# Optimization experiments

Hardware: AMD Instinct MI355X
Metric: run time of the kernel (lower is better)

## Reference

```python
import jax, jax.numpy as jnp
import numpy as np

B, IN, H = 8192, 1024, 1024


def setup_inputs() -> dict:
    key = jax.random.key(0)
    ks = jax.random.split(key, 16)
    s_in = 1.0 / np.sqrt(IN)
    s_h = 1.0 / np.sqrt(H)
    d = {}
    d['x'] = jax.random.normal(ks[0], (B, IN), jnp.float32)
    d['h'] = jax.random.normal(ks[1], (B, H), jnp.float32)
    d['c_prev'] = jax.random.normal(ks[2], (B, H), jnp.float32)
    d['W_fx'] = jax.random.normal(ks[3], (H, IN), jnp.float32) * s_in
    d['b_f'] = jax.random.normal(ks[4], (H,), jnp.float32) * s_in
    d['W_fh'] = jax.random.normal(ks[5], (H, H), jnp.float32) * s_h
    d['W_ix'] = jax.random.normal(ks[6], (H, IN), jnp.float32) * s_in
    d['b_i'] = jax.random.normal(ks[7], (H,), jnp.float32) * s_in
    d['W_ih'] = jax.random.normal(ks[8], (H, H), jnp.float32) * s_h
    d['W_gx'] = jax.random.normal(ks[9], (H, IN), jnp.float32) * s_in
    d['b_g'] = jax.random.normal(ks[10], (H,), jnp.float32) * s_in
    d['W_gh'] = jax.random.normal(ks[11], (H, H), jnp.float32) * s_h
    d['W_ox'] = jax.random.normal(ks[12], (H, IN), jnp.float32) * s_in
    d['b_o'] = jax.random.normal(ks[13], (H,), jnp.float32) * s_in
    d['W_oh'] = jax.random.normal(ks[14], (H, H), jnp.float32) * s_h
    return d


def reference(x, h, c_prev, W_fx, b_f, W_fh, W_ix, b_i, W_ih,
              W_gx, b_g, W_gh, W_ox, b_o, W_oh):
    # Concatenate the four x-projections and four h-projections into two
    # fused GEMMs (same math as the 8 separate nn.Linear calls).
    Wx = jnp.concatenate([W_ix, W_fx, W_gx, W_ox], axis=0)  # [4H, IN]
    Wh = jnp.concatenate([W_ih, W_fh, W_gh, W_oh], axis=0)  # [4H, H]
    bx = jnp.concatenate([b_i, b_f, b_g, b_o], axis=0)       # [4H]
    z = x @ Wx.T + h @ Wh.T + bx                              # [B, 4H]
    zi, zf, zg, zo = jnp.split(z, 4, axis=-1)
    i = jax.nn.sigmoid(zi)
    f = jax.nn.sigmoid(zf)
    g = jnp.tanh(zg)
    o = jax.nn.sigmoid(zo)
    c_next = f * c_prev + i * g
    h_next = o * jnp.tanh(c_next)
    return (h_next, c_next)
```

## Files before the change

kernel.cpp:

```cpp
#include <hip/hip_runtime.h>
#include <stdint.h>

typedef unsigned short ushort_t;
typedef __attribute__((ext_vector_type(8))) short short8;
typedef __attribute__((ext_vector_type(4))) float floatx4;

#define B_   8192
#define IN_  1024
#define H_   1024

#define XB_ELEMS   (B_ * IN_)
#define WB_ELEMS   (H_ * IN_)
#define WS_XB   0
#define WS_HB   XB_ELEMS
#define WS_WB   (2 * XB_ELEMS)

__device__ __forceinline__ ushort_t f2bf(float f) {
    union { float f; uint32_t i; } v; v.f = f;
    uint32_t r = (v.i + 0x7fffu + ((v.i >> 16) & 1u)) >> 16;
    return (ushort_t)r;
}
__device__ __forceinline__ float sigmoid_(float x) {
    return 1.0f / (1.0f + __expf(-x));
}
__device__ __forceinline__ float tanh_(float x) {
    float xc = fminf(fmaxf(x, -20.f), 20.f);
    float e = __expf(2.f * xc);
    return (e - 1.f) / (e + 1.f);
}

__device__ __forceinline__ void gll16(const ushort_t* gsrc, ushort_t* ldst) {
    __builtin_amdgcn_global_load_lds(
        (const __attribute__((address_space(1))) void*)gsrc,
        (__attribute__((address_space(3))) void*)ldst,
        16, 0, 0);
}

__global__ __launch_bounds__(256) void cvt_kernel(
    const float* __restrict__ X,   const float* __restrict__ Hin,
    const float* __restrict__ Wix, const float* __restrict__ Wfx,
    const float* __restrict__ Wgx, const float* __restrict__ Wox,
    const float* __restrict__ Wih, const float* __restrict__ Wfh,
    const float* __restrict__ Wgh, const float* __restrict__ Woh,
    ushort_t* __restrict__ ws)
{
    const int c = blockIdx.x * 256 + threadIdx.x;
    const float* src;
    ushort_t* dst;
    int off;
    if (c < 2097152) {
        const int t = c >> 20;
        src = t ? Hin : X;
        dst = ws + (t ? WS_HB : WS_XB);
        off = (c & 1048575) * 8;
    } else {
        const int cc = c - 2097152;
        const int s = cc >> 17;
        const float* w =
            s == 0 ? Wix : s == 1 ? Wfx : s == 2 ? Wgx : s == 3 ? Wox :
            s == 4 ? Wih : s == 5 ? Wfh : s == 6 ? Wgh : Woh;
        src = w;
        dst = ws + WS_WB + s * WB_ELEMS;
        off = (cc & 131071) * 8;
    }
    float4 f0 = *(const float4*)(src + off);
    float4 f1 = *(const float4*)(src + off + 4);
    short8 o;
    o[0] = (short)f2bf(f0.x); o[1] = (short)f2bf(f0.y);
    o[2] = (short)f2bf(f0.z); o[3] = (short)f2bf(f0.w);
    o[4] = (short)f2bf(f1.x); o[5] = (short)f2bf(f1.y);
    o[6] = (short)f2bf(f1.z); o[7] = (short)f2bf(f1.w);
    *(short8*)(dst + off) = o;
}

__global__ __launch_bounds__(256) void lstm_cell_kernel(
    const ushort_t* __restrict__ Xb,  const ushort_t* __restrict__ Hb,
    const ushort_t* __restrict__ Wb,
    const float* __restrict__ Cprev,
    const float* __restrict__ Bi, const float* __restrict__ Bf,
    const float* __restrict__ Bg, const float* __restrict__ Bo,
    float* __restrict__ Out)
{
    __shared__ __align__(16) ushort_t As[128 * 32];
    __shared__ __align__(16) ushort_t Bs[128 * 32];

    const int t   = threadIdx.x;
    const int bm0 = blockIdx.y * 128;
    const int j0  = blockIdx.x * 32;

    const int idx0 = t, idx1 = t + 256;
    const int rA0 = idx0 >> 2, kA0 = (idx0 & 3) * 8;
    const int rA1 = idx1 >> 2, kA1 = (idx1 & 3) * 8;

    const ushort_t* xA0 = Xb + (size_t)(bm0 + rA0) * IN_ + kA0;
    const ushort_t* xA1 = Xb + (size_t)(bm0 + rA1) * IN_ + kA1;
    const ushort_t* hA0 = Hb + (size_t)(bm0 + rA0) * H_  + kA0;
    const ushort_t* hA1 = Hb + (size_t)(bm0 + rA1) * H_  + kA1;

    const int g0 = (rA0 >> 4) & 3, g1 = (rA1 >> 4) & 3;
    const int jj0_ = j0 + ((rA0 >> 6) << 4) + (rA0 & 15);
    const int jj1_ = j0 + ((rA1 >> 6) << 4) + (rA1 & 15);
    const ushort_t* wx0 = Wb + (size_t)g0 * WB_ELEMS + (size_t)jj0_ * IN_ + kA0;
    const ushort_t* wx1 = Wb + (size_t)g1 * WB_ELEMS + (size_t)jj1_ * IN_ + kA1;
    const ushort_t* wh0 = Wb + (size_t)(4 + g0) * WB_ELEMS + (size_t)jj0_ * H_ + kA0;
    const ushort_t* wh1 = Wb + (size_t)(4 + g1) * WB_ELEMS + (size_t)jj1_ * H_ + kA1;

    ushort_t* ldsA0 = &As[idx0 * 8];
    ushort_t* ldsA1 = &As[idx1 * 8];
    ushort_t* ldsB0 = &Bs[idx0 * 8];
    ushort_t* ldsB1 = &Bs[idx1 * 8];

    const int lane = t & 63;
    const int w = t >> 6;
    const int lr = lane & 15, lk = lane >> 4;
    const int rowbase = (w >> 1) * 64;
    const int colhalf = w & 1;
    const int aoff = (rowbase + lr) * 32 + lk * 8;
    const int boff = (colhalf * 64 + lr) * 32 + lk * 8;

    floatx4 acc[4][4] = {};

    for (int phase = 0; phase < 2; ++phase) {
        const ushort_t* a0 = phase ? hA0 : xA0;
        const ushort_t* a1 = phase ? hA1 : xA1;
        const ushort_t* b0 = phase ? wh0 : wx0;
        const ushort_t* b1 = phase ? wh1 : wx1;
        for (int k0 = 0; k0 < 1024; k0 += 32) {
            gll16(a0, ldsA0);
            gll16(a1, ldsA1);
            gll16(b0, ldsB0);
            gll16(b1, ldsB1);
            a0 += 32; a1 += 32; b0 += 32; b1 += 32;
            __syncthreads();

            short8 af[4], bfr[4];
            #pragma unroll
            for (int rt = 0; rt < 4; ++rt)
                af[rt] = *(const short8*)(&As[aoff + rt * 512]);
            #pragma unroll
            for (int ct = 0; ct < 4; ++ct)
                bfr[ct] = *(const short8*)(&Bs[boff + ct * 512]);
            #pragma unroll
            for (int rt = 0; rt < 4; ++rt)
                #pragma unroll
                for (int ct = 0; ct < 4; ++ct)
                    acc[rt][ct] = __builtin_amdgcn_mfma_f32_16x16x32_bf16(
                        af[rt], bfr[ct], acc[rt][ct], 0, 0, 0);
            __syncthreads();
        }
    }

    const int j = j0 + colhalf * 16 + lr;
    const float bi = Bi[j], bff = Bf[j], bg = Bg[j], bo = Bo[j];

    #pragma unroll
    for (int rt = 0; rt < 4; ++rt) {
        #pragma unroll
        for (int reg = 0; reg < 4; ++reg) {
            const int m = bm0 + rowbase + rt * 16 + lk * 4 + reg;
            const float zi = acc[rt][0][reg] + bi;
            const float zf = acc[rt][1][reg] + bff;
            const float zg = acc[rt][2][reg] + bg;
            const float zo = acc[rt][3][reg] + bo;
            const float ig = sigmoid_(zi);
            const float fg = sigmoid_(zf);
            const float gg = tanh_(zg);
            const float og = sigmoid_(zo);
            const float cp = Cprev[(size_t)m * H_ + j];
            const float cn = fg * cp + ig * gg;
            const float hn = og * tanh_(cn);
            Out[(size_t)m * H_ + j] = hn;
            Out[(size_t)B_ * H_ + (size_t)m * H_ + j] = cn;
        }
    }
}

extern "C" void kernel_launch(void* const* d_in, const int* in_sizes, int n_in,
                              void* d_out, int out_size, void* d_ws, size_t ws_size,
                              hipStream_t stream)
{
    (void)in_sizes; (void)n_in; (void)out_size; (void)ws_size;
    const float* X   = (const float*)d_in[0];
    const float* Hin = (const float*)d_in[1];
    const float* Cp  = (const float*)d_in[2];
    const float* Wfx = (const float*)d_in[3];
    const float* Bf  = (const float*)d_in[4];
    const float* Wfh = (const float*)d_in[5];
    const float* Wix = (const float*)d_in[6];
    const float* Bi  = (const float*)d_in[7];
    const float* Wih = (const float*)d_in[8];
    const float* Wgx = (const float*)d_in[9];
    const float* Bg  = (const float*)d_in[10];
    const float* Wgh = (const float*)d_in[11];
    const float* Wox = (const float*)d_in[12];
    const float* Bo  = (const float*)d_in[13];
    const float* Woh = (const float*)d_in[14];
    float* Out = (float*)d_out;
    ushort_t* ws  = (ushort_t*)d_ws;

    cvt_kernel<<<dim3(12288), dim3(256), 0, stream>>>(
        X, Hin, Wix, Wfx, Wgx, Wox, Wih, Wfh, Wgh, Woh, ws);

    dim3 grid(H_ / 32, B_ / 128);
    lstm_cell_kernel<<<grid, dim3(256), 0, stream>>>(
        ws + WS_XB, ws + WS_HB, ws + WS_WB,
        Cp, Bi, Bf, Bg, Bo, Out);
}
```

Measured before the change: 344.9 us.

## Load fp32 activations directly into LDS and convert in-kernel, swizzle LDS

Removes the separate conversion of X and H to bf16, so the pre-pass only converts weights. The GEMM kernel streams fp32 activations straight into LDS with global_load_lds and truncates them to bf16 while building the MFMA fragments. Both the A and B LDS tiles now use a rotated (swizzled) layout to reduce bank conflicts. The cost is twice the A-tile global and LDS traffic per K step inside the GEMM. Rounding also changes from round-to-nearest to truncation for the activations.

```diff
diff --git a/kernel.cpp b/kernel.cpp
--- a/kernel.cpp
+++ b/kernel.cpp
@@ -9,11 +9,7 @@
 #define IN_  1024
 #define H_   1024
 
-#define XB_ELEMS   (B_ * IN_)
 #define WB_ELEMS   (H_ * IN_)
-#define WS_XB   0
-#define WS_HB   XB_ELEMS
-#define WS_WB   (2 * XB_ELEMS)
 
 __device__ __forceinline__ ushort_t f2bf(float f) {
     union { float f; uint32_t i; } v; v.f = f;
@@ -29,15 +25,14 @@
     return (e - 1.f) / (e + 1.f);
 }
 
-__device__ __forceinline__ void gll16(const ushort_t* gsrc, ushort_t* ldst) {
+__device__ __forceinline__ void gll16(const void* gsrc, void* ldst) {
     __builtin_amdgcn_global_load_lds(
         (const __attribute__((address_space(1))) void*)gsrc,
         (__attribute__((address_space(3))) void*)ldst,
         16, 0, 0);
 }
 
-__global__ __launch_bounds__(256) void cvt_kernel(
-    const float* __restrict__ X,   const float* __restrict__ Hin,
+__global__ __launch_bounds__(256) void cvt_w_kernel(
     const float* __restrict__ Wix, const float* __restrict__ Wfx,
     const float* __restrict__ Wgx, const float* __restrict__ Wox,
     const float* __restrict__ Wih, const float* __restrict__ Wfh,
@@ -45,24 +40,12 @@
     ushort_t* __restrict__ ws)
 {
     const int c = blockIdx.x * 256 + threadIdx.x;
-    const float* src;
-    ushort_t* dst;
-    int off;
-    if (c < 2097152) {
-        const int t = c >> 20;
-        src = t ? Hin : X;
-        dst = ws + (t ? WS_HB : WS_XB);
-        off = (c & 1048575) * 8;
-    } else {
-        const int cc = c - 2097152;
-        const int s = cc >> 17;
-        const float* w =
-            s == 0 ? Wix : s == 1 ? Wfx : s == 2 ? Wgx : s == 3 ? Wox :
-            s == 4 ? Wih : s == 5 ? Wfh : s == 6 ? Wgh : Woh;
-        src = w;
-        dst = ws + WS_WB + s * WB_ELEMS;
-        off = (cc & 131071) * 8;
-    }
+    const int s = c >> 17;
+    const float* src =
+        s == 0 ? Wix : s == 1 ? Wfx : s == 2 ? Wgx : s == 3 ? Wox :
+        s == 4 ? Wih : s == 5 ? Wfh : s == 6 ? Wgh : Woh;
+    ushort_t* dst = ws + (size_t)s * WB_ELEMS;
+    const int off = (c & 131071) * 8;
     float4 f0 = *(const float4*)(src + off);
     float4 f1 = *(const float4*)(src + off + 4);
     short8 o;
@@ -74,39 +57,44 @@
 }
 
 __global__ __launch_bounds__(256) void lstm_cell_kernel(
-    const ushort_t* __restrict__ Xb,  const ushort_t* __restrict__ Hb,
+    const float* __restrict__ Xf,  const float* __restrict__ Hf,
     const ushort_t* __restrict__ Wb,
     const float* __restrict__ Cprev,
     const float* __restrict__ Bi, const float* __restrict__ Bf,
     const float* __restrict__ Bg, const float* __restrict__ Bo,
     float* __restrict__ Out)
 {
-    __shared__ __align__(16) ushort_t As[128 * 32];
-    __shared__ __align__(16) ushort_t Bs[128 * 32];
+    __shared__ __align__(16) float    Asf[128 * 32];
+    __shared__ __align__(16) ushort_t Bs [128 * 32];
 
     const int t   = threadIdx.x;
     const int bm0 = blockIdx.y * 128;
     const int j0  = blockIdx.x * 32;
 
+    size_t offA[4];
+    #pragma unroll
+    for (int i = 0; i < 4; ++i) {
+        const int idx = t + 256 * i;
+        const int r = idx >> 3, p = idx & 7;
+        const int c = (p - r) & 7;
+        offA[i] = (size_t)(bm0 + r) * IN_ + c * 4;
+    }
+
     const int idx0 = t, idx1 = t + 256;
-    const int rA0 = idx0 >> 2, kA0 = (idx0 & 3) * 8;
-    const int rA1 = idx1 >> 2, kA1 = (idx1 & 3) * 8;
-
-    const ushort_t* xA0 = Xb + (size_t)(bm0 + rA0) * IN_ + kA0;
-    const ushort_t* xA1 = Xb + (size_t)(bm0 + rA1) * IN_ + kA1;
-    const ushort_t* hA0 = Hb + (size_t)(bm0 + rA0) * H_  + kA0;
-    const ushort_t* hA1 = Hb + (size_t)(bm0 + rA1) * H_  + kA1;
-
-    const int g0 = (rA0 >> 4) & 3, g1 = (rA1 >> 4) & 3;
-    const int jj0_ = j0 + ((rA0 >> 6) << 4) + (rA0 & 15);
-    const int jj1_ = j0 + ((rA1 >> 6) << 4) + (rA1 & 15);
-    const ushort_t* wx0 = Wb + (size_t)g0 * WB_ELEMS + (size_t)jj0_ * IN_ + kA0;
-    const ushort_t* wx1 = Wb + (size_t)g1 * WB_ELEMS + (size_t)jj1_ * IN_ + kA1;
-    const ushort_t* wh0 = Wb + (size_t)(4 + g0) * WB_ELEMS + (size_t)jj0_ * H_ + kA0;
-    const ushort_t* wh1 = Wb + (size_t)(4 + g1) * WB_ELEMS + (size_t)jj1_ * H_ + kA1;
-
-    ushort_t* ldsA0 = &As[idx0 * 8];
-    ushort_t* ldsA1 = &As[idx1 * 8];
+    const int vr0 = idx0 >> 2, pB0 = idx0 & 3, cB0 = (pB0 - (vr0 >> 1)) & 3;
+    const int vr1 = idx1 >> 2, pB1 = idx1 & 3, cB1 = (pB1 - (vr1 >> 1)) & 3;
+    const int g0 = (vr0 >> 4) & 3, g1 = (vr1 >> 4) & 3;
+    const int jj0_ = j0 + ((vr0 >> 6) << 4) + (vr0 & 15);
+    const int jj1_ = j0 + ((vr1 >> 6) << 4) + (vr1 & 15);
+    const ushort_t* wx0 = Wb + (size_t)g0 * WB_ELEMS + (size_t)jj0_ * IN_ + cB0 * 8;
+    const ushort_t* wx1 = Wb + (size_t)g1 * WB_ELEMS + (size_t)jj1_ * IN_ + cB1 * 8;
+    const ushort_t* wh0 = Wb + (size_t)(4 + g0) * WB_ELEMS + (size_t)jj0_ * H_ + cB0 * 8;
+    const ushort_t* wh1 = Wb + (size_t)(4 + g1) * WB_ELEMS + (size_t)jj1_ * H_ + cB1 * 8;
+
+    float*    ldsA0 = &Asf[(t      ) * 4];
+    float*    ldsA1 = &Asf[(t + 256) * 4];
+    float*    ldsA2 = &Asf[(t + 512) * 4];
+    float*    ldsA3 = &Asf[(t + 768) * 4];
     ushort_t* ldsB0 = &Bs[idx0 * 8];
     ushort_t* ldsB1 = &Bs[idx1 * 8];
 
@@ -115,31 +103,45 @@
     const int lr = lane & 15, lk = lane >> 4;
     const int rowbase = (w >> 1) * 64;
     const int colhalf = w & 1;
-    const int aoff = (rowbase + lr) * 32 + lk * 8;
-    const int boff = (colhalf * 64 + lr) * 32 + lk * 8;
 
     floatx4 acc[4][4] = {};
 
     for (int phase = 0; phase < 2; ++phase) {
-        const ushort_t* a0 = phase ? hA0 : xA0;
-        const ushort_t* a1 = phase ? hA1 : xA1;
+        const float* abase = phase ? Hf : Xf;
         const ushort_t* b0 = phase ? wh0 : wx0;
         const ushort_t* b1 = phase ? wh1 : wx1;
         for (int k0 = 0; k0 < 1024; k0 += 32) {
-            gll16(a0, ldsA0);
-            gll16(a1, ldsA1);
+            gll16(abase + offA[0] + k0, ldsA0);
+            gll16(abase + offA[1] + k0, ldsA1);
+            gll16(abase + offA[2] + k0, ldsA2);
+            gll16(abase + offA[3] + k0, ldsA3);
             gll16(b0, ldsB0);
             gll16(b1, ldsB1);
-            a0 += 32; a1 += 32; b0 += 32; b1 += 32;
+            b0 += 32; b1 += 32;
             __syncthreads();
 
             short8 af[4], bfr[4];
             #pragma unroll
-            for (int rt = 0; rt < 4; ++rt)
-                af[rt] = *(const short8*)(&As[aoff + rt * 512]);
+            for (int rt = 0; rt < 4; ++rt) {
+                const int r = rowbase + rt * 16 + lr;
+                const int p0 = (lk * 2 + r) & 7;
+                const int p1 = (lk * 2 + 1 + r) & 7;
+                union { float4 f; uint4 u; } q0, q1;
+                q0.f = *(const float4*)(&Asf[r * 32 + p0 * 4]);
+                q1.f = *(const float4*)(&Asf[r * 32 + p1 * 4]);
+                union { uint32_t u[4]; short8 s; } pk;
+                pk.u[0] = (q0.u.y & 0xffff0000u) | (q0.u.x >> 16);
+                pk.u[1] = (q0.u.w & 0xffff0000u) | (q0.u.z >> 16);
+                pk.u[2] = (q1.u.y & 0xffff0000u) | (q1.u.x >> 16);
+                pk.u[3] = (q1.u.w & 0xffff0000u) | (q1.u.z >> 16);
+                af[rt] = pk.s;
+            }
             #pragma unroll
-            for (int ct = 0; ct < 4; ++ct)
-                bfr[ct] = *(const short8*)(&Bs[boff + ct * 512]);
+            for (int ct = 0; ct < 4; ++ct) {
+                const int vr = colhalf * 64 + ct * 16 + lr;
+                const int p = (lk + (vr >> 1)) & 3;
+                bfr[ct] = *(const short8*)(&Bs[vr * 32 + p * 8]);
+            }
             #pragma unroll
             for (int rt = 0; rt < 4; ++rt)
                 #pragma unroll
@@ -198,11 +200,10 @@
     float* Out = (float*)d_out;
     ushort_t* ws  = (ushort_t*)d_ws;
 
-    cvt_kernel<<<dim3(12288), dim3(256), 0, stream>>>(
-        X, Hin, Wix, Wfx, Wgx, Wox, Wih, Wfh, Wgh, Woh, ws);
+    cvt_w_kernel<<<dim3(4096), dim3(256), 0, stream>>>(
+        Wix, Wfx, Wgx, Wox, Wih, Wfh, Wgh, Woh, ws);
 
     dim3 grid(H_ / 32, B_ / 128);
     lstm_cell_kernel<<<grid, dim3(256), 0, stream>>>(
-        ws + WS_XB, ws + WS_HB, ws + WS_WB,
-        Cp, Bi, Bf, Bg, Bo, Out);
-}
+        X, Hin, ws, Cp, Bi, Bf, Bg, Bo, Out);
+}
```

Measured after the change: 467.9 us. +35.7%, slower.
